# Kernel tuning notes

Measured on AMD Instinct MI355X. Metric: run time of the kernel, lower is better.

## Reference

```python
import jax, jax.numpy as jnp
import numpy as np

B, T, D, H = 32, 1024, 512, 256  # batch, seq_len, input_size, lstm hidden per direction (2H == D)


def _lstm_dir(x_tbd, W_ih, W_hh, b):
    """Single-direction LSTM over time-major input [T, B, D] -> hidden states [T, B, H].
    PyTorch gate order: i, f, g, o."""
    xg = jnp.einsum('tbd,gd->tbg', x_tbd, W_ih) + b  # precompute input projections [T,B,4H]
    h0 = jnp.zeros((x_tbd.shape[1], W_hh.shape[1]), x_tbd.dtype)

    def step(carry, xt):
        h, c = carry
        g = xt + h @ W_hh.T
        i, f, gg, o = jnp.split(g, 4, axis=-1)
        c = jax.nn.sigmoid(f) * c + jax.nn.sigmoid(i) * jnp.tanh(gg)
        h = jax.nn.sigmoid(o) * jnp.tanh(c)
        return (h, c), h

    _, hs = jax.lax.scan(step, (h0, h0), xg)
    return hs


def setup_inputs() -> dict:
    key = jax.random.key(0)
    ks = jax.random.split(key, 10)
    s = 0.05
    # padding mask: 1 (True) for padding positions, built from random valid lengths
    lengths = jax.random.randint(ks[1], (B,), T // 2, T)
    x_mask = jnp.arange(T)[None, :] >= lengths[:, None]  # bool [B, T]
    return {
        'x': jax.random.normal(ks[0], (B, T, D), jnp.float32),
        'x_mask': x_mask,
        'W_ih_f': jax.random.normal(ks[2], (4 * H, D), jnp.float32) * s,
        'W_hh_f': jax.random.normal(ks[3], (4 * H, H), jnp.float32) * s,
        'b_f': jnp.zeros((4 * H,), jnp.float32),
        'W_ih_b': jax.random.normal(ks[4], (4 * H, D), jnp.float32) * s,
        'W_hh_b': jax.random.normal(ks[5], (4 * H, H), jnp.float32) * s,
        'b_b': jnp.zeros((4 * H,), jnp.float32),
        'W_l': jax.random.normal(ks[6], (D, D), jnp.float32) * s,
    }


def reference(x, x_mask, W_ih_f, W_hh_f, b_f, W_ih_b, W_hh_b, b_b, W_l):
    # BiRNN encode: 1-layer bidirectional LSTM, concat directions -> [B, T, 2H] == [B, T, D]
    xt = jnp.swapaxes(x, 0, 1)  # [T, B, D]
    h_f = _lstm_dir(xt, W_ih_f, W_hh_f, b_f)
    h_b = _lstm_dir(xt[::-1], W_ih_b, W_hh_b, b_b)[::-1]
    xe = jnp.swapaxes(jnp.concatenate([h_f, h_b], axis=-1), 0, 1)  # [B, T, D]

    # Bilinear self-attention: L = (x W_l^T) x^T, mask padded query rows, softmax, weighted sum
    proj = xe @ W_l.T  # [B, T, D]
    L = jnp.einsum('bid,bjd->bij', proj, xe)  # [B, T, T]
    L = jnp.where(x_mask[:, :, None], jnp.float32(-1e30), L)
    A = jax.nn.softmax(L, axis=-1)
    return jnp.einsum('bij,bjd->bid', A, xe)  # [B, T, D]
```

## Files before the change

### kernel.cpp

```cpp
#include <hip/hip_runtime.h>
#include <math.h>

#define T_SEQ 1024
#define B_SZ  32
#define D_SZ  512
#define H_SZ  256

typedef unsigned short u16;
typedef short v8bf __attribute__((ext_vector_type(8)));
typedef float v4f  __attribute__((ext_vector_type(4)));

__device__ __forceinline__ unsigned int f2bf(float f)
{
    unsigned int u = __float_as_uint(f);
    return (u + 0x7fffu + ((u >> 16) & 1u)) >> 16;
}
__device__ __forceinline__ u16 f2bfu(float f)
{
    unsigned int u = __float_as_uint(f);
    return (u16)((u + 0x7fffu + ((u >> 16) & 1u)) >> 16);
}
__device__ __forceinline__ float bfu2f(u16 h)
{
    return __uint_as_float(((unsigned int)h) << 16);
}

__device__ __forceinline__ void gload_lds16(const void* g, void* l)
{
    __builtin_amdgcn_global_load_lds(
        (const __attribute__((address_space(1))) void*)g,
        (__attribute__((address_space(3))) void*)l,
        16, 0, 0);
}

__device__ __forceinline__ void pinv(uint4& w)
{
    asm volatile("" : "+v"(w.x), "+v"(w.y), "+v"(w.z), "+v"(w.w));
}

__device__ __forceinline__ float tanh_fast(float x)
{
    float xc = fminf(fmaxf(x, -30.f), 30.f);
    float e = __expf(-2.f * xc);
    return (1.f - e) / (1.f + e);
}

#define BM 64
#define BN 64
#define BK 16

__global__ __launch_bounds__(256)
void gemm_nt(const float* __restrict__ A, const float* __restrict__ W,
             const float* __restrict__ bias, float* __restrict__ C,
             int M, int N, int K,
             long long sA, long long sW, long long sC)
{
    int z = blockIdx.z;
    A += (size_t)z * sA; W += (size_t)z * sW; C += (size_t)z * sC;
    int n0 = blockIdx.x * BN;
    int m0 = blockIdx.y * BM;
    int tid = threadIdx.x;
    int tm = tid >> 4, tn = tid & 15;

    __shared__ float As[BK][BM + 4];
    __shared__ float Ws[BK][BN + 4];

    float acc[4][4] = {};

    int lc = tid & 15;
    int lr = tid >> 4;

    for (int k0 = 0; k0 < K; k0 += BK) {
        #pragma unroll
        for (int i = 0; i < 4; ++i) {
            int r = lr + 16 * i;
            As[lc][r] = A[(size_t)(m0 + r) * K + k0 + lc];
            Ws[lc][r] = W[(size_t)(n0 + r) * K + k0 + lc];
        }
        __syncthreads();
        #pragma unroll
        for (int kk = 0; kk < BK; ++kk) {
            float4 a4 = *(const float4*)&As[kk][tm * 4];
            float4 b4 = *(const float4*)&Ws[kk][tn * 4];
            float a[4] = {a4.x, a4.y, a4.z, a4.w};
            float b[4] = {b4.x, b4.y, b4.z, b4.w};
            #pragma unroll
            for (int i = 0; i < 4; ++i)
                #pragma unroll
                for (int j = 0; j < 4; ++j)
                    acc[i][j] = fmaf(a[i], b[j], acc[i][j]);
        }
        __syncthreads();
    }

    float bb[4] = {0.f, 0.f, 0.f, 0.f};
    if (bias) {
        #pragma unroll
        for (int j = 0; j < 4; ++j) bb[j] = bias[n0 + tn * 4 + j];
    }
    #pragma unroll
    for (int i = 0; i < 4; ++i) {
        int m = m0 + tm * 4 + i;
        float4 o;
        o.x = acc[i][0] + bb[0];
        o.y = acc[i][1] + bb[1];
        o.z = acc[i][2] + bb[2];
        o.w = acc[i][3] + bb[3];
        *(float4*)&C[(size_t)m * N + n0 + tn * 4] = o;
    }
}

__global__ __launch_bounds__(256)
void gemm_nn(const float* __restrict__ A, const float* __restrict__ B,
             float* __restrict__ C, int M, int N, int K,
             long long sA, long long sB, long long sC)
{
    int z = blockIdx.z;
    A += (size_t)z * sA; B += (size_t)z * sB; C += (size_t)z * sC;
    int n0 = blockIdx.x * BN;
    int m0 = blockIdx.y * BM;
    int tid = threadIdx.x;
    int tm = tid >> 4, tn = tid & 15;

    __shared__ float As[BK][BM + 4];
    __shared__ float Bs[BK][BN + 4];

    float acc[4][4] = {};

    int lc = tid & 15;
    int lr = tid >> 4;
    int br = tid >> 6;
    int bc = tid & 63;

    for (int k0 = 0; k0 < K; k0 += BK) {
        #pragma unroll
        for (int i = 0; i < 4; ++i) {
            int r = lr + 16 * i;
            As[lc][r] = A[(size_t)(m0 + r) * K + k0 + lc];
        }
        #pragma unroll
        for (int i = 0; i < 4; ++i) {
            int r = br + 4 * i;
            Bs[r][bc] = B[(size_t)(k0 + r) * N + n0 + bc];
        }
        __syncthreads();
        #pragma unroll
        for (int kk = 0; kk < BK; ++kk) {
            float4 a4 = *(const float4*)&As[kk][tm * 4];
            float4 b4 = *(const float4*)&Bs[kk][tn * 4];
            float a[4] = {a4.x, a4.y, a4.z, a4.w};
            float b[4] = {b4.x, b4.y, b4.z, b4.w};
            #pragma unroll
            for (int i = 0; i < 4; ++i)
                #pragma unroll
                for (int j = 0; j < 4; ++j)
                    acc[i][j] = fmaf(a[i], b[j], acc[i][j]);
        }
        __syncthreads();
    }
    #pragma unroll
    for (int i = 0; i < 4; ++i) {
        int m = m0 + tm * 4 + i;
        float4 o;
        o.x = acc[i][0]; o.y = acc[i][1]; o.z = acc[i][2]; o.w = acc[i][3];
        *(float4*)&C[(size_t)m * N + n0 + tn * 4] = o;
    }
}

template<int EPI>
__global__ __launch_bounds__(256)
void gemm_ms(const u16* __restrict__ Ah, const u16* __restrict__ Al,
             const u16* __restrict__ Bh, const u16* __restrict__ Bl,
             const float* __restrict__ bias,
             float* __restrict__ C, u16* __restrict__ Chi, u16* __restrict__ Clo,
             int M, int N, int K,
             long long sA, long long sB, long long sC)
{
    int z = blockIdx.z;
    Ah += (size_t)z * sA; Al += (size_t)z * sA;
    Bh += (size_t)z * sB; Bl += (size_t)z * sB;
    int n0 = blockIdx.x * 128;
    int m0 = blockIdx.y * 128;
    int t  = threadIdx.x;
    int lane = t & 63, wid = t >> 6;

    __shared__ u16 sA_h[128 * 32];
    __shared__ u16 sA_l[128 * 32];
    __shared__ u16 sB_h[128 * 32];
    __shared__ u16 sB_l[128 * 32];

    int wm = (wid & 1) << 6;
    int wn = (wid >> 1) << 6;
    int fr = lane & 15;
    int g  = lane >> 4;

    v4f acc[4][4];
    #pragma unroll
    for (int i = 0; i < 4; ++i)
        #pragma unroll
        for (int j = 0; j < 4; ++j)
            acc[i][j] = (v4f){0.f, 0.f, 0.f, 0.f};

    int s0 = t;
    int s1 = t + 256;
    int r0 = s0 >> 2, gl0 = (s0 & 3) ^ ((s0 >> 3) & 3);
    int r1 = s1 >> 2, gl1 = (s1 & 3) ^ ((s1 >> 3) & 3);
    int lb0 = (wid << 6) << 3;
    int lb1 = ((wid << 6) + 256) << 3;

    for (int k0 = 0; k0 < K; k0 += 32) {
        size_t gA0 = (size_t)(m0 + r0) * K + k0 + gl0 * 8;
        size_t gA1 = (size_t)(m0 + r1) * K + k0 + gl1 * 8;
        size_t gB0 = (size_t)(n0 + r0) * K + k0 + gl0 * 8;
        size_t gB1 = (size_t)(n0 + r1) * K + k0 + gl1 * 8;
        gload_lds16(Ah + gA0, sA_h + lb0);
        gload_lds16(Ah + gA1, sA_h + lb1);
        gload_lds16(Al + gA0, sA_l + lb0);
        gload_lds16(Al + gA1, sA_l + lb1);
        gload_lds16(Bh + gB0, sB_h + lb0);
        gload_lds16(Bh + gB1, sB_h + lb1);
        gload_lds16(Bl + gB0, sB_l + lb0);
        gload_lds16(Bl + gB1, sB_l + lb1);
        __syncthreads();

        #pragma unroll
        for (int pass = 0; pass < 3; ++pass) {
            const u16* sB_p = (pass == 2) ? sB_l : sB_h;
            const u16* sA_p = (pass == 1) ? sA_l : sA_h;
            v8bf bf[4];
            #pragma unroll
            for (int ni = 0; ni < 4; ++ni) {
                int r = wn + ni * 16 + fr;
                bf[ni] = *(const v8bf*)&sB_p[r * 32 + ((g ^ ((r >> 1) & 3)) << 3)];
            }
            #pragma unroll
            for (int mi = 0; mi < 4; ++mi) {
                int r = wm + mi * 16 + fr;
                v8bf af = *(const v8bf*)&sA_p[r * 32 + ((g ^ ((r >> 1) & 3)) << 3)];
                #pragma unroll
                for (int ni = 0; ni < 4; ++ni)
                    acc[mi][ni] = __builtin_amdgcn_mfma_f32_16x16x32_bf16(
                        af, bf[ni], acc[mi][ni], 0, 0, 0);
            }
        }
        __syncthreads();
    }

    int ocol = lane & 15;
    int orow = (lane >> 4) << 2;
    if (EPI == 1) {
        #pragma unroll
        for (int mi = 0; mi < 4; ++mi) {
            #pragma unroll
            for (int rr = 0; rr < 4; ++rr) {
                int m = m0 + wm + mi * 16 + orow + rr;
                #pragma unroll
                for (int ni = 0; ni < 4; ++ni) {
                    int n = n0 + wn + ni * 16 + ocol;
                    float v = acc[mi][ni][rr];
                    u16 h = f2bfu(v);
                    Chi[(size_t)m * N + n] = h;
                    Clo[(size_t)m * N + n] = f2bfu(v - bfu2f(h));
                }
            }
        }
    } else {
        float* Cz = C + (size_t)z * sC;
        float bb[4] = {0.f, 0.f, 0.f, 0.f};
        if (bias) {
            #pragma unroll
            for (int ni = 0; ni < 4; ++ni) bb[ni] = bias[n0 + wn + ni * 16 + ocol];
        }
        #pragma unroll
        for (int mi = 0; mi < 4; ++mi) {
            #pragma unroll
            for (int rr = 0; rr < 4; ++rr) {
                int m = m0 + wm + mi * 16 + orow + rr;
                #pragma unroll
                for (int ni = 0; ni < 4; ++ni) {
                    int n = n0 + wn + ni * 16 + ocol;
                    Cz[(size_t)m * N + n] = acc[mi][ni][rr] + bb[ni];
                }
            }
        }
    }
}

__global__ __launch_bounds__(256)
void convert_split(const float4* __restrict__ in,
                   ushort4* __restrict__ hi, ushort4* __restrict__ lo)
{
    size_t i = (size_t)blockIdx.x * 256 + threadIdx.x;
    float4 v = in[i];
    ushort4 h, l;
    h.x = f2bfu(v.x); l.x = f2bfu(v.x - bfu2f(h.x));
    h.y = f2bfu(v.y); l.y = f2bfu(v.y - bfu2f(h.y));
    h.z = f2bfu(v.z); l.z = f2bfu(v.z - bfu2f(h.z));
    h.w = f2bfu(v.w); l.w = f2bfu(v.w - bfu2f(h.w));
    hi[i] = h;
    lo[i] = l;
}

__global__ __launch_bounds__(256)
void transpose_split_xe(const float* __restrict__ xe,
                        u16* __restrict__ Th, u16* __restrict__ Tl)
{
    int b = blockIdx.z;
    const float* X = xe + (size_t)b * T_SEQ * D_SZ;
    u16* TH = Th + (size_t)b * T_SEQ * D_SZ;
    u16* TL = Tl + (size_t)b * T_SEQ * D_SZ;
    int t0 = blockIdx.x << 5, d0 = blockIdx.y << 5;

    __shared__ float tile[32][33];
    int tx = threadIdx.x & 31, ty = threadIdx.x >> 5;

    #pragma unroll
    for (int i = 0; i < 4; ++i)
        tile[ty + (i << 3)][tx] = X[(size_t)(t0 + ty + (i << 3)) * D_SZ + d0 + tx];
    __syncthreads();
    #pragma unroll
    for (int i = 0; i < 4; ++i) {
        int dd = ty + (i << 3);
        float v = tile[tx][dd];
        u16 h = f2bfu(v);
        TH[(size_t)(d0 + dd) * T_SEQ + t0 + tx] = h;
        TL[(size_t)(d0 + dd) * T_SEQ + t0 + tx] = f2bfu(v - bfu2f(h));
    }
}

__global__ __launch_bounds__(256)
void pack_whh_bf16(const float* __restrict__ Wf, const float* __restrict__ Wb,
                   uint4* __restrict__ Wpf, uint4* __restrict__ Wpb)
{
    int idx = blockIdx.x * 256 + threadIdx.x;
    int u = idx & (H_SZ - 1);
    int p = idx >> 8;
    uint4 a, b;
    unsigned int* pa = (unsigned int*)&a;
    unsigned int* pb = (unsigned int*)&b;
    #pragma unroll
    for (int g = 0; g < 4; ++g) {
        size_t row = (size_t)(g * H_SZ + u) * H_SZ;
        pa[g] = f2bf(Wf[row + 2 * p]) | (f2bf(Wf[row + 2 * p + 1]) << 16);
        pb[g] = f2bf(Wb[row + 2 * p]) | (f2bf(Wb[row + 2 * p + 1]) << 16);
    }
    Wpf[idx] = a;
    Wpb[idx] = b;
}

__global__ __launch_bounds__(1024, 4)
void lstm_bf16(const float* __restrict__ xgA, const uint4* __restrict__ WpA,
               const float* __restrict__ xgB, const uint4* __restrict__ WpB,
               float* __restrict__ xe, int d0, int fused)
{
    int i = blockIdx.x;
    int b, dir;
    if (fused) {
        int j = i & 7, m = i >> 3;
        dir = j >> 2;
        b   = (j & 3) * 8 + m;
    } else {
        b   = (i & 3) * 8 + (i >> 2);
        dir = d0;
    }
    const float* xg = dir ? xgB : xgA;
    const uint4* Wp = dir ? WpB : WpA;

    int tid   = threadIdx.x;
    int u     = tid & (H_SZ - 1);
    int slice = tid >> 8;
    int p0    = slice << 5;

    __shared__ float  hs[H_SZ];
    __shared__ float4 part[4][H_SZ];

    uint4 wres[16];
    {
        const uint4* wb = Wp + (size_t)p0 * H_SZ + u;
        #pragma unroll
        for (int q = 0; q < 16; ++q) wres[q] = wb[q * H_SZ];
        #pragma unroll
        for (int q = 0; q < 16; ++q) pinv(wres[q]);
    }
    const uint4* wstream = Wp + (size_t)(p0 + 16) * H_SZ + u;

    if (tid < H_SZ) hs[tid] = 0.f;
    float c = 0.f;
    __syncthreads();

    for (int s = 0; s < T_SEQ; ++s) {
        int t = dir ? (T_SEQ - 1 - s) : s;

        float xi = 0.f, xf = 0.f, xgv = 0.f, xo = 0.f;
        if (tid < H_SZ) {
            const float* row = xg + ((size_t)b * T_SEQ + t) * (4 * H_SZ);
            xi  = row[u];
            xf  = row[H_SZ + u];
            xgv = row[2 * H_SZ + u];
            xo  = row[3 * H_SZ + u];
        }

        uint4 pf[6];
        #pragma unroll
        for (int q = 0; q < 6; ++q)
            pf[q] = wstream[(size_t)((q + s) & 15) * H_SZ];

        float4 acc; acc.x = 0.f; acc.y = 0.f; acc.z = 0.f; acc.w = 0.f;

        #define DOT_PAIR(WQ, P)                                             \
        {                                                                   \
            float2 hp = *(const float2*)&hs[2 * (P)];                       \
            const unsigned int* wc = (const unsigned int*)&(WQ);            \
            _Pragma("unroll")                                               \
            for (int g = 0; g < 4; ++g) {                                   \
                float wlo = __uint_as_float(wc[g] << 16);                   \
                float whi = __uint_as_float(wc[g] & 0xffff0000u);           \
                ((float*)&acc)[g] =                                         \
                    fmaf(whi, hp.y, fmaf(wlo, hp.x, ((float*)&acc)[g]));    \
            }                                                               \
        }

        #pragma unroll
        for (int q = 0; q < 16; ++q) {
            DOT_PAIR(wres[q], p0 + q);
        }
        #pragma unroll
        for (int q = 0; q < 16; ++q) {
            uint4 wq = pf[q % 6];
            if (q + 6 < 16)
                pf[q % 6] = wstream[(size_t)((q + 6 + s) & 15) * H_SZ];
            int qr = (q + s) & 15;
            DOT_PAIR(wq, p0 + 16 + qr);
        }
        #undef DOT_PAIR

        part[slice][u] = acc;
        __syncthreads();

        if (tid < H_SZ) {
            float4 pp0 = part[0][u], pp1 = part[1][u], pp2 = part[2][u], pp3 = part[3][u];
            float ai = xi  + pp0.x + pp1.x + pp2.x + pp3.x;
            float af = xf  + pp0.y + pp1.y + pp2.y + pp3.y;
            float ag = xgv + pp0.z + pp1.z + pp2.z + pp3.z;
            float ao = xo  + pp0.w + pp1.w + pp2.w + pp3.w;
            float ig = 1.f / (1.f + __expf(-ai));
            float fg = 1.f / (1.f + __expf(-af));
            float gg = tanh_fast(ag);
            float og = 1.f / (1.f + __expf(-ao));
            c = fg * c + ig * gg;
            float h = og * tanh_fast(c);
            hs[u] = h;
            xe[((size_t)b * T_SEQ + t) * D_SZ + dir * H_SZ + u] = h;
        }
        __syncthreads();
    }
}

__global__ __launch_bounds__(256)
void softmax_rows(float* __restrict__ L, const void* __restrict__ maskraw)
{
    const unsigned char* mu8 = (const unsigned char*)maskraw;
    const int*           mi32 = (const int*)maskraw;
    bool layout_u8 = (mu8[1023] != 0);

    int lane = threadIdx.x & 63;
    int wid  = threadIdx.x >> 6;
    int row  = (blockIdx.x << 2) + wid;
    float* p = L + (size_t)row * T_SEQ;

    int mval = layout_u8 ? (int)mu8[row] : mi32[row];

    if (mval != 0) {
        const float inv = 1.0f / (float)T_SEQ;
        for (int j = lane; j < T_SEQ; j += 64) p[j] = inv;
        return;
    }

    float v[16];
    float m = -1e30f;
    #pragma unroll
    for (int u = 0; u < 16; ++u) {
        v[u] = p[lane + (u << 6)];
        m = fmaxf(m, v[u]);
    }
    #pragma unroll
    for (int s = 32; s; s >>= 1) m = fmaxf(m, __shfl_xor(m, s, 64));

    float sum = 0.f;
    #pragma unroll
    for (int u = 0; u < 16; ++u) {
        v[u] = __expf(v[u] - m);
        sum += v[u];
    }
    #pragma unroll
    for (int s = 32; s; s >>= 1) sum += __shfl_xor(sum, s, 64);

    float inv = 1.0f / sum;
    #pragma unroll
    for (int u = 0; u < 16; ++u) p[lane + (u << 6)] = v[u] * inv;
}

extern "C" void kernel_launch(void* const* d_in, const int* in_sizes, int n_in,
                              void* d_out, int out_size, void* d_ws, size_t ws_size,
                              hipStream_t stream)
{
    const float* x     = (const float*)d_in[0];
    const void*  xmask = d_in[1];
    const float* Wih_f = (const float*)d_in[2];
    const float* Whh_f = (const float*)d_in[3];
    const float* b_f   = (const float*)d_in[4];
    const float* Wih_b = (const float*)d_in[5];
    const float* Whh_b = (const float*)d_in[6];
    const float* b_b   = (const float*)d_in[7];
    const float* W_l   = (const float*)d_in[8];
    float* out = (float*)d_out;

    char* ws = (char*)d_ws;
    const size_t MB1 = (size_t)1 << 20;
    const size_t SZ_XE = (size_t)B_SZ * T_SEQ * D_SZ * sizeof(float);
    const size_t SZ_XG = (size_t)B_SZ * T_SEQ * 4 * H_SZ * sizeof(float);
    bool fused = ws_size >= SZ_XE + 2 * SZ_XG;

    const int MT = B_SZ * T_SEQ;
    const long long sTD = (long long)T_SEQ * D_SZ;
    const long long sTT = (long long)T_SEQ * T_SEQ;

    uint4* Wpf = (uint4*)d_out;
    uint4* Wpb = (uint4*)d_out + 128 * H_SZ;

    pack_whh_bf16<<<dim3((128 * H_SZ) / 256), dim3(256), 0, stream>>>(
        Whh_f, Whh_b, Wpf, Wpb);

    if (fused) {
        u16* x_hi  = (u16*)(ws);
        u16* x_lo  = (u16*)(ws + 32 * MB1);
        float* xg_f = (float*)(ws + 64 * MB1);
        float* xg_b = (float*)(ws + 192 * MB1);
        float* xe   = (float*)(ws);
        u16* xe_hi = (u16*)(ws + 64 * MB1);
        u16* xe_lo = (u16*)(ws + 96 * MB1);
        u16* pj_hi = (u16*)(ws + 128 * MB1);
        u16* pj_lo = (u16*)(ws + 160 * MB1);
        float* L   = (float*)(ws + 192 * MB1);
        u16* xT_hi = pj_hi;
        u16* xT_lo = pj_lo;
        u16* L_hi  = (u16*)(ws);
        u16* L_lo  = (u16*)(ws + 64 * MB1);

        u16* Wihf_hi = (u16*)((char*)d_out + 1 * MB1);
        u16* Wihf_lo = (u16*)((char*)d_out + 2 * MB1);
        u16* Wihb_hi = (u16*)((char*)d_out + 3 * MB1);
        u16* Wihb_lo = (u16*)((char*)d_out + 4 * MB1);
        u16* Wl_hi   = (u16*)((char*)d_out + 5 * MB1);
        u16* Wl_lo   = (u16*)((char*)d_out + 5 * MB1 + (MB1 >> 1));

        convert_split<<<dim3((MT * D_SZ) / 1024), dim3(256), 0, stream>>>(
            (const float4*)x, (ushort4*)x_hi, (ushort4*)x_lo);
        convert_split<<<dim3((4 * H_SZ * D_SZ) / 1024), dim3(256), 0, stream>>>(
            (const float4*)Wih_f, (ushort4*)Wihf_hi, (ushort4*)Wihf_lo);
        convert_split<<<dim3((4 * H_SZ * D_SZ) / 1024), dim3(256), 0, stream>>>(
            (const float4*)Wih_b, (ushort4*)Wihb_hi, (ushort4*)Wihb_lo);
        convert_split<<<dim3((D_SZ * D_SZ) / 1024), dim3(256), 0, stream>>>(
            (const float4*)W_l, (ushort4*)Wl_hi, (ushort4*)Wl_lo);

        gemm_ms<0><<<dim3((4 * H_SZ) / 128, MT / 128, 1), dim3(256), 0, stream>>>(
            x_hi, x_lo, Wihf_hi, Wihf_lo, b_f, xg_f, nullptr, nullptr,
            MT, 4 * H_SZ, D_SZ, 0, 0, 0);
        gemm_ms<0><<<dim3((4 * H_SZ) / 128, MT / 128, 1), dim3(256), 0, stream>>>(
            x_hi, x_lo, Wihb_hi, Wihb_lo, b_b, xg_b, nullptr, nullptr,
            MT, 4 * H_SZ, D_SZ, 0, 0, 0);

        lstm_bf16<<<dim3(2 * B_SZ), dim3(1024), 0, stream>>>(
            xg_f, Wpf, xg_b, Wpb, xe, 0, 1);

        convert_split<<<dim3((MT * D_SZ) / 1024), dim3(256), 0, stream>>>(
            (const float4*)xe, (ushort4*)xe_hi, (ushort4*)xe_lo);

        gemm_ms<1><<<dim3(D_SZ / 128, MT / 128, 1), dim3(256), 0, stream>>>(
            xe_hi, xe_lo, Wl_hi, Wl_lo, nullptr, nullptr, pj_hi, pj_lo,
            MT, D_SZ, D_SZ, 0, 0, 0);

        gemm_ms<0><<<dim3(T_SEQ / 128, T_SEQ / 128, B_SZ), dim3(256), 0, stream>>>(
            pj_hi, pj_lo, xe_hi, xe_lo, nullptr, L, nullptr, nullptr,
            T_SEQ, T_SEQ, D_SZ, sTD, sTD, sTT);

        softmax_rows<<<dim3(MT / 4), dim3(256), 0, stream>>>(L, xmask);

        transpose_split_xe<<<dim3(T_SEQ / 32, D_SZ / 32, B_SZ), dim3(256), 0, stream>>>(
            xe, xT_hi, xT_lo);

        convert_split<<<dim3((MT * T_SEQ) / 1024), dim3(256), 0, stream>>>(
            (const float4*)L, (ushort4*)L_hi, (ushort4*)L_lo);

        gemm_ms<0><<<dim3(D_SZ / 128, T_SEQ / 128, B_SZ), dim3(256), 0, stream>>>(
            L_hi, L_lo, xT_hi, xT_lo, nullptr, out, nullptr, nullptr,
            T_SEQ, D_SZ, T_SEQ, sTT, sTD, sTD);
    } else {
        float* xe   = (float*)(ws);
        float* xg_f = (float*)(ws + SZ_XE);
        float* xg_b = xg_f;
        float* L    = xg_f;
        float* proj = out;

        gemm_nt<<<dim3((4 * H_SZ) / BN, MT / BM, 1), dim3(256), 0, stream>>>(
            x, Wih_f, b_f, xg_f, MT, 4 * H_SZ, D_SZ, 0, 0, 0);
        lstm_bf16<<<dim3(B_SZ), dim3(1024), 0, stream>>>(
            xg_f, Wpf, xg_f, Wpf, xe, 0, 0);
        gemm_nt<<<dim3((4 * H_SZ) / BN, MT / BM, 1), dim3(256), 0, stream>>>(
            x, Wih_b, b_b, xg_b, MT, 4 * H_SZ, D_SZ, 0, 0, 0);
        lstm_bf16<<<dim3(B_SZ), dim3(1024), 0, stream>>>(
            xg_b, Wpb, xg_b, Wpb, xe, 1, 0);

        gemm_nt<<<dim3(D_SZ / BN, MT / BM, 1), dim3(256), 0, stream>>>(
            xe, W_l, nullptr, proj, MT, D_SZ, D_SZ, 0, 0, 0);
        gemm_nt<<<dim3(T_SEQ / BN, T_SEQ / BM, B_SZ), dim3(256), 0, stream>>>(
            proj, xe, nullptr, L, T_SEQ, T_SEQ, D_SZ, sTD, sTD, sTT);
        softmax_rows<<<dim3(MT / 4), dim3(256), 0, stream>>>(L, xmask);
        gemm_nn<<<dim3(D_SZ / BN, T_SEQ / BM, B_SZ), dim3(256), 0, stream>>>(
            L, xe, out, T_SEQ, D_SZ, T_SEQ, sTT, sTD, sTD);
    }
}
```

Before: 16.82 ms.

## Replace scalar LSTM recurrence with MFMA batched kernel over 16 sequences per block

Adds a new LSTM recurrence kernel, used on the fused path. Each workgroup handles 16 batch rows of one direction and computes the h·W_hh^T product with bf16 MFMA instructions. The hidden state is kept in LDS as a swizzled bf16 hi/lo split to preserve accuracy, and W_hh is packed row-wise to bf16 and read from global/L2 every step instead of being held in registers. This replaces 64 workgroups each doing scalar FMAs for one sequence with only 4 workgroups, cutting per-step FMA work and sync count per sequence. The trade-off is that each step re-streams about half a megabyte of weights per CU and most CUs sit idle. The old kernel's register pinning and prefetch ring are also simplified.

```diff
diff --git a/kernel.cpp b/kernel.cpp
--- a/kernel.cpp
+++ b/kernel.cpp
@@ -31,11 +31,6 @@
         (const __attribute__((address_space(1))) void*)g,
         (__attribute__((address_space(3))) void*)l,
         16, 0, 0);
-}
-
-__device__ __forceinline__ void pinv(uint4& w)
-{
-    asm volatile("" : "+v"(w.x), "+v"(w.y), "+v"(w.z), "+v"(w.w));
 }
 
 __device__ __forceinline__ float tanh_fast(float x)
@@ -348,7 +343,123 @@
     Wpb[idx] = b;
 }
 
-__global__ __launch_bounds__(1024, 4)
+__global__ __launch_bounds__(256)
+void pack_w_rows(const float4* __restrict__ Wf, const float4* __restrict__ Wb,
+                 ushort4* __restrict__ Of, ushort4* __restrict__ Ob)
+{
+    size_t i = (size_t)blockIdx.x * 256 + threadIdx.x;
+    float4 a = Wf[i], b = Wb[i];
+    ushort4 oa, ob;
+    oa.x = f2bfu(a.x); oa.y = f2bfu(a.y); oa.z = f2bfu(a.z); oa.w = f2bfu(a.w);
+    ob.x = f2bfu(b.x); ob.y = f2bfu(b.y); ob.z = f2bfu(b.z); ob.w = f2bfu(b.w);
+    Of[i] = oa;
+    Ob[i] = ob;
+}
+
+__global__ __launch_bounds__(512, 2)
+void lstm_mfma(const float* __restrict__ xgA, const u16* __restrict__ WA,
+               const float* __restrict__ xgB, const u16* __restrict__ WB,
+               float* __restrict__ xe)
+{
+    int bi  = blockIdx.x;
+    int dir = bi >> 1;
+    int b0  = (bi & 1) * 16;
+    const float* xg = dir ? xgB : xgA;
+    const u16*  W   = dir ? WB : WA;
+
+    int tid  = threadIdx.x;
+    int lane = tid & 63, wv = tid >> 6;
+    int wn   = wv << 7;
+    int fr   = lane & 15;
+    int kg   = lane >> 4;
+
+    __shared__ u16  hHi[16 * 256];
+    __shared__ u16  hLo[16 * 256];
+    __shared__ float gate[16][1024 + 4];
+
+    for (int i = tid; i < 16 * 256; i += 512) { hHi[i] = 0; hLo[i] = 0; }
+
+    const u16* bp[8];
+    #pragma unroll
+    for (int ni = 0; ni < 8; ++ni)
+        bp[ni] = W + (size_t)(wn + ni * 16 + fr) * 256 + kg * 8;
+
+    int u  = tid & 255;
+    int bh = tid >> 8;
+    float c8[8];
+    #pragma unroll
+    for (int j = 0; j < 8; ++j) c8[j] = 0.f;
+
+    __syncthreads();
+
+    for (int s = 0; s < T_SEQ; ++s) {
+        int t = dir ? (T_SEQ - 1 - s) : s;
+
+        float pxi[8], pxf[8], pxg[8], pxo[8];
+        #pragma unroll
+        for (int j = 0; j < 8; ++j) {
+            int bl = bh * 8 + j;
+            const float* row = xg + ((size_t)(b0 + bl) * T_SEQ + t) * (4 * H_SZ);
+            pxi[j] = row[u];
+            pxf[j] = row[256 + u];
+            pxg[j] = row[512 + u];
+            pxo[j] = row[768 + u];
+        }
+
+        v4f accH[8], accL[8];
+        #pragma unroll
+        for (int ni = 0; ni < 8; ++ni) {
+            accH[ni] = (v4f){0.f, 0.f, 0.f, 0.f};
+            accL[ni] = (v4f){0.f, 0.f, 0.f, 0.f};
+        }
+
+        #pragma unroll
+        for (int ks = 0; ks < 8; ++ks) {
+            int aoff = fr * 512 + ((((ks << 2) + kg) ^ (fr & 7)) << 4);
+            v8bf aH = *(const v8bf*)((const char*)hHi + aoff);
+            v8bf aL = *(const v8bf*)((const char*)hLo + aoff);
+            #pragma unroll
+            for (int ni = 0; ni < 8; ++ni) {
+                v8bf bf = *(const v8bf*)(bp[ni] + ks * 32);
+                accH[ni] = __builtin_amdgcn_mfma_f32_16x16x32_bf16(aH, bf, accH[ni], 0, 0, 0);
+                accL[ni] = __builtin_amdgcn_mfma_f32_16x16x32_bf16(aL, bf, accL[ni], 0, 0, 0);
+            }
+        }
+
+        int orow = kg << 2;
+        #pragma unroll
+        for (int ni = 0; ni < 8; ++ni) {
+            #pragma unroll
+            for (int r = 0; r < 4; ++r)
+                gate[orow + r][wn + ni * 16 + fr] = accH[ni][r] + accL[ni][r];
+        }
+        __syncthreads();
+
+        #pragma unroll
+        for (int j = 0; j < 8; ++j) {
+            int bl = bh * 8 + j;
+            float ai = pxi[j] + gate[bl][u];
+            float af = pxf[j] + gate[bl][256 + u];
+            float ag = pxg[j] + gate[bl][512 + u];
+            float ao = pxo[j] + gate[bl][768 + u];
+            float ig = 1.f / (1.f + __expf(-ai));
+            float fg = 1.f / (1.f + __expf(-af));
+            float gv = tanh_fast(ag);
+            float og = 1.f / (1.f + __expf(-ao));
+            c8[j] = fg * c8[j] + ig * gv;
+            float hv = og * tanh_fast(c8[j]);
+            xe[((size_t)(b0 + bl) * T_SEQ + t) * D_SZ + dir * H_SZ + u] = hv;
+            u16 hh = f2bfu(hv);
+            u16 hl = f2bfu(hv - bfu2f(hh));
+            int hoff = bl * 512 + ((((u >> 3) ^ (bl & 7)) << 4)) + ((u & 7) << 1);
+            *(u16*)((char*)hHi + hoff) = hh;
+            *(u16*)((char*)hLo + hoff) = hl;
+        }
+        __syncthreads();
+    }
+}
+
+__global__ __launch_bounds__(1024)
 void lstm_bf16(const float* __restrict__ xgA, const uint4* __restrict__ WpA,
                const float* __restrict__ xgB, const uint4* __restrict__ WpB,
                float* __restrict__ xe, int d0, int fused)
@@ -379,8 +490,6 @@
         const uint4* wb = Wp + (size_t)p0 * H_SZ + u;
         #pragma unroll
         for (int q = 0; q < 16; ++q) wres[q] = wb[q * H_SZ];
-        #pragma unroll
-        for (int q = 0; q < 16; ++q) pinv(wres[q]);
     }
     const uint4* wstream = Wp + (size_t)(p0 + 16) * H_SZ + u;
 
@@ -399,11 +508,6 @@
             xgv = row[2 * H_SZ + u];
             xo  = row[3 * H_SZ + u];
         }
-
-        uint4 pf[6];
-        #pragma unroll
-        for (int q = 0; q < 6; ++q)
-            pf[q] = wstream[(size_t)((q + s) & 15) * H_SZ];
 
         float4 acc; acc.x = 0.f; acc.y = 0.f; acc.z = 0.f; acc.w = 0.f;
 
@@ -426,10 +530,8 @@
         }
         #pragma unroll
         for (int q = 0; q < 16; ++q) {
-            uint4 wq = pf[q % 6];
-            if (q + 6 < 16)
-                pf[q % 6] = wstream[(size_t)((q + 6 + s) & 15) * H_SZ];
             int qr = (q + s) & 15;
+            uint4 wq = wstream[(size_t)qr * H_SZ];
             DOT_PAIR(wq, p0 + 16 + qr);
         }
         #undef DOT_PAIR
@@ -524,12 +626,6 @@
     const int MT = B_SZ * T_SEQ;
     const long long sTD = (long long)T_SEQ * D_SZ;
     const long long sTT = (long long)T_SEQ * T_SEQ;
-
-    uint4* Wpf = (uint4*)d_out;
-    uint4* Wpb = (uint4*)d_out + 128 * H_SZ;
-
-    pack_whh_bf16<<<dim3((128 * H_SZ) / 256), dim3(256), 0, stream>>>(
-        Whh_f, Whh_b, Wpf, Wpb);
 
     if (fused) {
         u16* x_hi  = (u16*)(ws);
@@ -547,6 +643,8 @@
         u16* L_hi  = (u16*)(ws);
         u16* L_lo  = (u16*)(ws + 64 * MB1);
 
+        u16* WB_f    = (u16*)d_out;
+        u16* WB_b    = (u16*)((char*)d_out + (MB1 >> 1));
         u16* Wihf_hi = (u16*)((char*)d_out + 1 * MB1);
         u16* Wihf_lo = (u16*)((char*)d_out + 2 * MB1);
         u16* Wihb_hi = (u16*)((char*)d_out + 3 * MB1);
@@ -554,6 +652,9 @@
         u16* Wl_hi   = (u16*)((char*)d_out + 5 * MB1);
         u16* Wl_lo   = (u16*)((char*)d_out + 5 * MB1 + (MB1 >> 1));
 
+        pack_w_rows<<<dim3((4 * H_SZ * H_SZ) / 1024), dim3(256), 0, stream>>>(
+            (const float4*)Whh_f, (const float4*)Whh_b,
+            (ushort4*)WB_f, (ushort4*)WB_b);
         convert_split<<<dim3((MT * D_SZ) / 1024), dim3(256), 0, stream>>>(
             (const float4*)x, (ushort4*)x_hi, (ushort4*)x_lo);
         convert_split<<<dim3((4 * H_SZ * D_SZ) / 1024), dim3(256), 0, stream>>>(
@@ -570,8 +671,8 @@
             x_hi, x_lo, Wihb_hi, Wihb_lo, b_b, xg_b, nullptr, nullptr,
             MT, 4 * H_SZ, D_SZ, 0, 0, 0);
 
-        lstm_bf16<<<dim3(2 * B_SZ), dim3(1024), 0, stream>>>(
-            xg_f, Wpf, xg_b, Wpb, xe, 0, 1);
+        lstm_mfma<<<dim3(4), dim3(512), 0, stream>>>(
+            xg_f, WB_f, xg_b, WB_b, xe);
 
         convert_split<<<dim3((MT * D_SZ) / 1024), dim3(256), 0, stream>>>(
             (const float4*)xe, (ushort4*)xe_hi, (ushort4*)xe_lo);
@@ -596,12 +697,16 @@
             L_hi, L_lo, xT_hi, xT_lo, nullptr, out, nullptr, nullptr,
             T_SEQ, D_SZ, T_SEQ, sTT, sTD, sTD);
     } else {
+        uint4* Wpf = (uint4*)d_out;
+        uint4* Wpb = (uint4*)d_out + 128 * H_SZ;
         float* xe   = (float*)(ws);
         float* xg_f = (float*)(ws + SZ_XE);
         float* xg_b = xg_f;
         float* L    = xg_f;
         float* proj = out;
 
+        pack_whh_bf16<<<dim3((128 * H_SZ) / 256), dim3(256), 0, stream>>>(
+            Whh_f, Whh_b, Wpf, Wpb);
         gemm_nt<<<dim3((4 * H_SZ) / BN, MT / BM, 1), dim3(256), 0, stream>>>(
             x, Wih_f, b_f, xg_f, MT, 4 * H_SZ, D_SZ, 0, 0, 0);
         lstm_bf16<<<dim3(B_SZ), dim3(1024), 0, stream>>>(
```

Result: no change. 17.00 ms (+1.1%).
